# Kernel tuning notes

Measured on AMD Instinct MI355X. Metric: run time of the kernel, lower is better.

## Reference

```python
import jax, jax.numpy as jnp
import numpy as np

BETA = 0.25


def setup_inputs() -> dict:
    key = jax.random.key(0)
    k1, k2 = jax.random.split(key)
    z = jax.random.normal(k1, (16, 256, 32, 32), dtype=jnp.float32)
    n_e, e_dim = 8192, 256
    # torch init: uniform(-1/n_e, 1/n_e)
    codebook = jax.random.uniform(k2, (n_e, e_dim), dtype=jnp.float32,
                                  minval=-1.0 / n_e, maxval=1.0 / n_e)
    return {"z": z, "codebook": codebook}


def reference(z, codebook):
    # z: [B, C, H, W] -> [B, H, W, C]
    z_perm = jnp.transpose(z, (0, 2, 3, 1))
    B, H, W, C = z_perm.shape
    flat = z_perm.reshape(-1, C)  # [N, e_dim]
    distances = (jnp.sum(flat ** 2, axis=1, keepdims=True)
                 + jnp.sum(codebook ** 2, axis=1)
                 - 2.0 * jnp.matmul(flat, codebook.T))  # [N, n_e]
    indices = jnp.argmin(distances, axis=1)  # [N]
    quant = codebook[indices].reshape(z_perm.shape)  # [B, H, W, C]
    loss = (BETA * jnp.mean((jax.lax.stop_gradient(quant) - z_perm) ** 2)
            + jnp.mean((quant - jax.lax.stop_gradient(z_perm)) ** 2))
    # straight-through estimator
    quant = z_perm + jax.lax.stop_gradient(quant - z_perm)
    quant = jnp.transpose(quant, (0, 3, 1, 2))  # back to [B, C, H, W]
    return quant, loss, indices
```

## Files before the change

### kernel.cpp

```cpp
#include <hip/hip_runtime.h>
#include <stdint.h>

#define N_ROWS 16384
#define N_E    8192
#define EDIM   256
#define QELEMS 4194304
#define NCHUNK 256

using f32x4  = __attribute__((ext_vector_type(4))) float;
using bf16x8 = __attribute__((ext_vector_type(8))) short;

__device__ __forceinline__ unsigned int f2ord(float f) {
    unsigned int u = __float_as_uint(f);
    return (u & 0x80000000u) ? ~u : (u | 0x80000000u);
}
__device__ __forceinline__ float ord2f(unsigned int o) {
    unsigned int u = (o & 0x80000000u) ? (o & 0x7fffffffu) : ~o;
    return __uint_as_float(u);
}
__device__ __forceinline__ unsigned long long shfl_xor_u64(unsigned long long v, int m) {
    int lo = __shfl_xor((int)(unsigned int)(v & 0xffffffffull), m);
    int hi = __shfl_xor((int)(unsigned int)(v >> 32), m);
    return ((unsigned long long)(unsigned int)hi << 32) | (unsigned long long)(unsigned int)lo;
}
__device__ __forceinline__ unsigned short f2bf(float f) {
    unsigned int u = __float_as_uint(f);
    u += 0x7fffu + ((u >> 16) & 1u);
    return (unsigned short)(u >> 16);
}

__global__ void vq_rownorm(const float* __restrict__ z, float* __restrict__ Crow,
                           float* __restrict__ Mrow) {
    int r = blockIdx.x * blockDim.x + threadIdx.x;
    if (r >= N_ROWS) return;
    int b = r >> 10, hw = r & 1023;
    const float* p = z + ((size_t)b << 18) + hw;
    double s0 = 0.0, s1 = 0.0, s2 = 0.0, s3 = 0.0;
    float sa = 0.0f;
    #pragma unroll 4
    for (int c = 0; c < EDIM; c += 4) {
        float v0 = p[(size_t)(c + 0) << 10];
        float v1 = p[(size_t)(c + 1) << 10];
        float v2 = p[(size_t)(c + 2) << 10];
        float v3 = p[(size_t)(c + 3) << 10];
        float w0 = v0 * v0, w1 = v1 * v1, w2 = v2 * v2, w3 = v3 * v3;
        s0 += (double)w0; s1 += (double)w1; s2 += (double)w2; s3 += (double)w3;
        sa += fabsf(v0) + fabsf(v1) + fabsf(v2) + fabsf(v3);
    }
    Crow[r] = (float)((s0 + s1) + (s2 + s3));
    Mrow[r] = 1.6e-4f + 3.0e-6f * sa;
}

__global__ void vq_transpose(const float* __restrict__ z, float* __restrict__ Zt,
                             unsigned short* __restrict__ Zth) {
    __shared__ float tile[64][65];
    const int t = threadIdx.x;
    const int ct = blockIdx.x, rt = blockIdx.y;
    const int tr = t & 63, tc = t >> 6;
    #pragma unroll
    for (int i = 0; i < 16; ++i) {
        int c_l = i * 4 + tc;
        int r = rt * 64 + tr;
        int c = ct * 64 + c_l;
        tile[tr][c_l] = z[(((size_t)(r >> 10) * 256 + c) << 10) + (r & 1023)];
    }
    __syncthreads();
    const int c = ct * 64 + tr;
    const int kt = c >> 5, lkq = (c >> 3) & 3, k0 = c & 7;
    #pragma unroll
    for (int i = 0; i < 16; ++i) {
        int r_l = i * 4 + tc;
        int r = rt * 64 + r_l;
        float v = tile[r_l][tr];
        Zt[(size_t)r * EDIM + c] = v;
        size_t off = (((size_t)(r >> 4) * 8 + kt) * 64 + lkq * 16 + (r & 15)) * 8 + k0;
        Zth[off] = f2bf(v);
    }
}

__global__ void vq_cbsplit(const float* __restrict__ cb, unsigned short* __restrict__ cbh) {
    const int t = threadIdx.x;
    const int nt = blockIdx.x, ktb = blockIdx.y;
    const int nl0 = t >> 4, kq = t & 15;
    #pragma unroll
    for (int i = 0; i < 8; ++i) {
        int nl = i * 16 + nl0;
        int n = nt * 128 + nl;
        int k = ktb * 64 + kq * 4;
        float4 v = *(const float4*)(cb + (size_t)n * EDIM + k);
        ushort4 H;
        H.x = f2bf(v.x); H.y = f2bf(v.y); H.z = f2bf(v.z); H.w = f2bf(v.w);
        int kt = k >> 5, lkq = (k >> 3) & 3, k0 = k & 7;
        size_t off = (((size_t)(n >> 4) * 8 + kt) * 64 + lkq * 16 + (n & 15)) * 8 + k0;
        *(ushort4*)(cbh + off) = H;
    }
}

__global__ __launch_bounds__(512, 2) void vq_gemm(
    const unsigned short* __restrict__ Zth, const unsigned short* __restrict__ cbh,
    unsigned int* __restrict__ part)
{
    const int t = threadIdx.x;
    const int lane = t & 63, w = t >> 6;
    const int bid = blockIdx.x;
    const int rg0 = bid * 4;
    const int row0 = bid * 64;
    const unsigned short* gA = Zth + (size_t)lane * 8;
    const unsigned short* pB = cbh + (size_t)lane * 8;

    bf16x8 A[4][8];
    #pragma unroll
    for (int i = 0; i < 4; ++i)
        #pragma unroll
        for (int kt = 0; kt < 8; ++kt)
            A[i][kt] = *(const bf16x8*)(gA + (((size_t)(rg0 + i) * 8 + kt) << 9));

    const int cfw = w * 64;
    bf16x8 bc[8], bn[8];

#define LDB(dst, cf) { _Pragma("unroll") \
    for (int kt_ = 0; kt_ < 8; ++kt_) \
        (dst)[kt_] = *(const bf16x8*)(pB + (((size_t)(cf) * 8 + kt_) << 9)); }

    LDB(bc, cfw);

    #pragma unroll 1
    for (int ch = 0; ch < 32; ++ch) {
        #pragma unroll
        for (int i = 0; i < 4; ++i)
            #pragma unroll
            for (int kt = 0; kt < 8; ++kt)
                asm volatile("" : "+v"(A[i][kt]));

        const int gch = w * 32 + ch;
        f32x4 acc0[4], acc1[4];
        #pragma unroll
        for (int i = 0; i < 4; ++i) {
            acc0[i] = (f32x4){0.f, 0.f, 0.f, 0.f};
            acc1[i] = (f32x4){0.f, 0.f, 0.f, 0.f};
        }
        LDB(bn, cfw + ch * 2 + 1);
        __builtin_amdgcn_s_setprio(1);
        #pragma unroll
        for (int kt = 0; kt < 8; ++kt) {
            acc0[0] = __builtin_amdgcn_mfma_f32_16x16x32_bf16(bc[kt], A[0][kt], acc0[0], 0, 0, 0);
            acc0[1] = __builtin_amdgcn_mfma_f32_16x16x32_bf16(bc[kt], A[1][kt], acc0[1], 0, 0, 0);
            acc0[2] = __builtin_amdgcn_mfma_f32_16x16x32_bf16(bc[kt], A[2][kt], acc0[2], 0, 0, 0);
            acc0[3] = __builtin_amdgcn_mfma_f32_16x16x32_bf16(bc[kt], A[3][kt], acc0[3], 0, 0, 0);
        }
        __builtin_amdgcn_s_setprio(0);
        LDB(bc, (ch < 31) ? (cfw + ch * 2 + 2) : cfw);
        __builtin_amdgcn_s_setprio(1);
        #pragma unroll
        for (int kt = 0; kt < 8; ++kt) {
            acc1[0] = __builtin_amdgcn_mfma_f32_16x16x32_bf16(bn[kt], A[0][kt], acc1[0], 0, 0, 0);
            acc1[1] = __builtin_amdgcn_mfma_f32_16x16x32_bf16(bn[kt], A[1][kt], acc1[1], 0, 0, 0);
            acc1[2] = __builtin_amdgcn_mfma_f32_16x16x32_bf16(bn[kt], A[2][kt], acc1[2], 0, 0, 0);
            acc1[3] = __builtin_amdgcn_mfma_f32_16x16x32_bf16(bn[kt], A[3][kt], acc1[3], 0, 0, 0);
        }
        __builtin_amdgcn_s_setprio(0);
        #pragma unroll
        for (int i = 0; i < 4; ++i) {
            float m0 = fmaxf(acc0[i][0], acc1[i][0]);
            float m1 = fmaxf(acc0[i][1], acc1[i][1]);
            float m2 = fmaxf(acc0[i][2], acc1[i][2]);
            float m3 = fmaxf(acc0[i][3], acc1[i][3]);
            float v = fmaxf(fmaxf(m0, m1), fmaxf(m2, m3));
            v = fmaxf(v, __shfl_xor(v, 16));
            v = fmaxf(v, __shfl_xor(v, 32));
            if (lane < 16)
                part[(size_t)gch * N_ROWS + row0 + i * 16 + lane] = f2ord(v);
        }
    }
#undef LDB
}

__global__ void vq_qualify(const unsigned int* __restrict__ part,
                           const float* __restrict__ Mrow,
                           unsigned int* __restrict__ uthr)
{
    int row = blockIdx.x * 256 + threadIdx.x;
    unsigned int umax = 0u;
    for (int c = 0; c < NCHUNK; ++c) {
        unsigned int u = part[(size_t)c * N_ROWS + row];
        umax = (u > umax) ? u : umax;
    }
    float thr = ord2f(umax) - 0.5f * Mrow[row];
    uthr[row] = f2ord(thr);
}

__global__ __launch_bounds__(256, 1) void vq_recheck(
    const float* __restrict__ Zt, const float* __restrict__ cb,
    const float* __restrict__ Crow, const unsigned int* __restrict__ part,
    const unsigned int* __restrict__ uthr, unsigned long long* __restrict__ keys)
{
    __shared__ float cbt[32 * 256];
    __shared__ int lrows[N_ROWS];
    __shared__ int lcount;
    const int t = threadIdx.x;
    const int chunk = blockIdx.x;
    if (t == 0) lcount = 0;
    {
        int col = t >> 3, kq = t & 7;
        const float* src = cb + (size_t)(chunk * 32 + col) * EDIM + kq * 32;
        #pragma unroll
        for (int j = 0; j < 8; ++j) {
            float4 v = *(const float4*)(src + j * 4);
            int k4 = kq * 8 + j;
            *(float4*)&cbt[col * 256 + (((unsigned)(k4 ^ (col & 7))) << 2)] = v;
        }
    }
    __syncthreads();
    for (int r0 = 0; r0 < N_ROWS; r0 += 256) {
        int row = r0 + t;
        if (part[(size_t)chunk * N_ROWS + row] >= uthr[row]) {
            int pos = atomicAdd(&lcount, 1);
            lrows[pos] = row;
        }
    }
    __syncthreads();
    const int cnt = lcount;
    const int cg = t & 7, rl = t >> 3;
    for (int i0 = 0; i0 < cnt; i0 += 32) {
        int li = i0 + rl;
        bool valid = li < cnt;
        int row = lrows[valid ? li : (cnt - 1)];
        const float* zp = Zt + (size_t)row * EDIM;
        float a0 = 0.f, a1 = 0.f, a2 = 0.f, a3 = 0.f;
        #pragma unroll 8
        for (int k4 = 0; k4 < 64; ++k4) {
            float4 zv = *(const float4*)(zp + k4 * 4);
            int g = ((unsigned)(k4 ^ cg)) << 2;
            float4 b0 = *(const float4*)&cbt[(cg +  0) * 256 + g];
            float4 b1 = *(const float4*)&cbt[(cg +  8) * 256 + g];
            float4 b2 = *(const float4*)&cbt[(cg + 16) * 256 + g];
            float4 b3 = *(const float4*)&cbt[(cg + 24) * 256 + g];
            a0 = fmaf(zv.x, b0.x, a0); a0 = fmaf(zv.y, b0.y, a0);
            a0 = fmaf(zv.z, b0.z, a0); a0 = fmaf(zv.w, b0.w, a0);
            a1 = fmaf(zv.x, b1.x, a1); a1 = fmaf(zv.y, b1.y, a1);
            a1 = fmaf(zv.z, b1.z, a1); a1 = fmaf(zv.w, b1.w, a1);
            a2 = fmaf(zv.x, b2.x, a2); a2 = fmaf(zv.y, b2.y, a2);
            a2 = fmaf(zv.z, b2.z, a2); a2 = fmaf(zv.w, b2.w, a2);
            a3 = fmaf(zv.x, b3.x, a3); a3 = fmaf(zv.y, b3.y, a3);
            a3 = fmaf(zv.z, b3.z, a3); a3 = fmaf(zv.w, b3.w, a3);
        }
        float Cr = Crow[row];
        int colbase = chunk * 32;
        unsigned long long best;
        {
            unsigned long long k0 = ((unsigned long long)f2ord(Cr - 2.0f * a0) << 32) | (unsigned int)(colbase + cg);
            unsigned long long k1 = ((unsigned long long)f2ord(Cr - 2.0f * a1) << 32) | (unsigned int)(colbase + cg + 8);
            unsigned long long k2 = ((unsigned long long)f2ord(Cr - 2.0f * a2) << 32) | (unsigned int)(colbase + cg + 16);
            unsigned long long k3 = ((unsigned long long)f2ord(Cr - 2.0f * a3) << 32) | (unsigned int)(colbase + cg + 24);
            best = (k0 < k1) ? k0 : k1;
            best = (k2 < best) ? k2 : best;
            best = (k3 < best) ? k3 : best;
        }
        #pragma unroll
        for (int m = 1; m <= 4; m <<= 1) {
            unsigned long long o = shfl_xor_u64(best, m);
            best = (o < best) ? o : best;
        }
        if (cg == 0 && valid) atomicMin(&keys[row], best);
    }
}

__global__ void vq_finalize(const float* __restrict__ z, const float* __restrict__ cb,
                            const unsigned long long* __restrict__ keys,
                            float* __restrict__ out_q, float* __restrict__ out_idx,
                            double* __restrict__ accum)
{
    __shared__ float qld[64][257];
    __shared__ int sIdx[64];
    const int t = threadIdx.x;
    const int r0 = blockIdx.x * 64;
    const int b = r0 >> 10, hw0 = r0 & 1023;
    if (t < 64) {
        unsigned int idx = (unsigned int)(keys[r0 + t] & 0xffffffffull);
        sIdx[t] = (int)idx;
        out_idx[r0 + t] = (float)idx;
    }
    __syncthreads();
    {
        int i = t >> 2, q4 = t & 3;
        const float* src = cb + (size_t)sIdx[i] * EDIM;
        #pragma unroll
        for (int j = 0; j < 16; ++j)
            *(float4*)&qld[i][j * 16 + q4 * 4] = *(const float4*)(src + j * 16 + q4 * 4);
    }
    __syncthreads();
    const int hw_l = t & 63, cg = t >> 6;
    double p = 0.0;
    #pragma unroll 4
    for (int j = 0; j < 64; ++j) {
        int c = cg * 64 + j;
        float q  = qld[hw_l][c];
        size_t o = (((size_t)(b * 256 + c)) << 10) + hw0 + hw_l;
        float zv = z[o];
        float d  = q - zv;
        out_q[o] = zv + d;
        p += (double)d * (double)d;
    }
    #pragma unroll
    for (int m = 32; m >= 1; m >>= 1) p += __shfl_down(p, m);
    __shared__ double wsum[4];
    if ((t & 63) == 0) wsum[t >> 6] = p;
    __syncthreads();
    if (t == 0)
        atomicAdd(accum, (wsum[0] + wsum[1]) + (wsum[2] + wsum[3]));
}

__global__ void vq_loss(const double* __restrict__ accum, float* __restrict__ out_loss) {
    out_loss[0] = (float)(1.25 * (accum[0] / (double)QELEMS));
}

extern "C" void kernel_launch(void* const* d_in, const int* in_sizes, int n_in,
                              void* d_out, int out_size, void* d_ws, size_t ws_size,
                              hipStream_t stream) {
    const float* z  = (const float*)d_in[0];
    const float* cb = (const float*)d_in[1];
    float* out = (float*)d_out;

    char* ws = (char*)d_ws;
    unsigned long long* keys = (unsigned long long*)(ws + 0);
    float*  Crow  = (float*)(ws + 131072);
    float*  Mrow  = (float*)(ws + 196608);
    unsigned int* uthr = (unsigned int*)(ws + 262144);
    double* accum = (double*)(ws + 327680);
    unsigned int* part = (unsigned int*)(ws + 331776);
    float*  Zt    = (float*)(ws + 17108992);
    unsigned short* Zth = (unsigned short*)(ws + 33886208);
    unsigned short* cbh = (unsigned short*)(ws + 42274816);

    hipMemsetAsync(keys, 0xFF, (size_t)N_ROWS * 8, stream);
    hipMemsetAsync(accum, 0, 8, stream);

    vq_rownorm  <<<N_ROWS / 256, 256, 0, stream>>>(z, Crow, Mrow);
    vq_transpose<<<dim3(4, 256), 256, 0, stream>>>(z, Zt, Zth);
    vq_cbsplit  <<<dim3(64, 4), 256, 0, stream>>>(cb, cbh);
    vq_gemm     <<<256, 512, 0, stream>>>(Zth, cbh, part);
    vq_qualify  <<<N_ROWS / 256, 256, 0, stream>>>(part, Mrow, uthr);
    vq_recheck  <<<NCHUNK, 256, 0, stream>>>(Zt, cb, Crow, part, uthr, keys);
    vq_finalize <<<N_ROWS / 64, 256, 0, stream>>>(z, cb, keys, out, out + QELEMS + 1, accum);
    vq_loss     <<<1, 1, 0, stream>>>(accum, out + QELEMS);
}
```

Baseline: 183.0 us.

## Build per-chunk candidate lists in qualify and split recheck across four blocks per chunk

The qualify kernel now computes each row's threshold and scans all chunks, appending qualifying row indices as 16-bit values to per-chunk global lists through global atomics. Recheck no longer scans all 16384 rows per chunk into a 64KB shared list; it reads the prebuilt list and splits each chunk's candidates across four blocks, with a launch bound that allows three blocks per CU. This removes the per-chunk full scan of part/uthr and the heavy shared memory use, which should raise occupancy and parallelism. The cost is a second pass over part in qualify, contended global atomics on the per-chunk counters, and reuse of the Zth buffer for the lists after the GEMM has consumed it.

New measurement: 349.9 us. 1.91x slower.

```diff
diff --git a/kernel.cpp b/kernel.cpp
--- a/kernel.cpp
+++ b/kernel.cpp
@@ -177,7 +177,8 @@
 
 __global__ void vq_qualify(const unsigned int* __restrict__ part,
                            const float* __restrict__ Mrow,
-                           unsigned int* __restrict__ uthr)
+                           int* __restrict__ counts,
+                           unsigned short* __restrict__ lists16)
 {
     int row = blockIdx.x * 256 + threadIdx.x;
     unsigned int umax = 0u;
@@ -186,20 +187,24 @@
         umax = (u > umax) ? u : umax;
     }
     float thr = ord2f(umax) - 0.5f * Mrow[row];
-    uthr[row] = f2ord(thr);
-}
-
-__global__ __launch_bounds__(256, 1) void vq_recheck(
+    unsigned int uthrv = f2ord(thr);
+    for (int c = 0; c < NCHUNK; ++c)
+        if (part[(size_t)c * N_ROWS + row] >= uthrv) {
+            int pos = atomicAdd(&counts[c], 1);
+            lists16[(size_t)c * N_ROWS + pos] = (unsigned short)row;
+        }
+}
+
+__global__ __launch_bounds__(256, 3) void vq_recheck(
     const float* __restrict__ Zt, const float* __restrict__ cb,
-    const float* __restrict__ Crow, const unsigned int* __restrict__ part,
-    const unsigned int* __restrict__ uthr, unsigned long long* __restrict__ keys)
+    const float* __restrict__ Crow, const int* __restrict__ counts,
+    const unsigned short* __restrict__ lists16, unsigned long long* __restrict__ keys)
 {
     __shared__ float cbt[32 * 256];
-    __shared__ int lrows[N_ROWS];
-    __shared__ int lcount;
-    const int t = threadIdx.x;
-    const int chunk = blockIdx.x;
-    if (t == 0) lcount = 0;
+    const int t = threadIdx.x;
+    const int chunk = blockIdx.x >> 2, sub = blockIdx.x & 3;
+    const int cnt = counts[chunk];
+    if (cnt == 0 || sub * 32 >= cnt) return;
     {
         int col = t >> 3, kq = t & 7;
         const float* src = cb + (size_t)(chunk * 32 + col) * EDIM + kq * 32;
@@ -211,20 +216,12 @@
         }
     }
     __syncthreads();
-    for (int r0 = 0; r0 < N_ROWS; r0 += 256) {
-        int row = r0 + t;
-        if (part[(size_t)chunk * N_ROWS + row] >= uthr[row]) {
-            int pos = atomicAdd(&lcount, 1);
-            lrows[pos] = row;
-        }
-    }
-    __syncthreads();
-    const int cnt = lcount;
     const int cg = t & 7, rl = t >> 3;
-    for (int i0 = 0; i0 < cnt; i0 += 32) {
+    const unsigned short* lst = lists16 + (size_t)chunk * N_ROWS;
+    for (int i0 = sub * 32; i0 < cnt; i0 += 128) {
         int li = i0 + rl;
         bool valid = li < cnt;
-        int row = lrows[valid ? li : (cnt - 1)];
+        int row = lst[valid ? li : (cnt - 1)];
         const float* zp = Zt + (size_t)row * EDIM;
         float a0 = 0.f, a1 = 0.f, a2 = 0.f, a3 = 0.f;
         #pragma unroll 8
@@ -325,22 +322,24 @@
     unsigned long long* keys = (unsigned long long*)(ws + 0);
     float*  Crow  = (float*)(ws + 131072);
     float*  Mrow  = (float*)(ws + 196608);
-    unsigned int* uthr = (unsigned int*)(ws + 262144);
     double* accum = (double*)(ws + 327680);
+    int*    counts = (int*)(ws + 327688);
     unsigned int* part = (unsigned int*)(ws + 331776);
     float*  Zt    = (float*)(ws + 17108992);
     unsigned short* Zth = (unsigned short*)(ws + 33886208);
     unsigned short* cbh = (unsigned short*)(ws + 42274816);
+    unsigned short* lists16 = Zth;
 
     hipMemsetAsync(keys, 0xFF, (size_t)N_ROWS * 8, stream);
     hipMemsetAsync(accum, 0, 8, stream);
+    hipMemsetAsync(counts, 0, 1024, stream);
 
     vq_rownorm  <<<N_ROWS / 256, 256, 0, stream>>>(z, Crow, Mrow);
     vq_transpose<<<dim3(4, 256), 256, 0, stream>>>(z, Zt, Zth);
     vq_cbsplit  <<<dim3(64, 4), 256, 0, stream>>>(cb, cbh);
     vq_gemm     <<<256, 512, 0, stream>>>(Zth, cbh, part);
-    vq_qualify  <<<N_ROWS / 256, 256, 0, stream>>>(part, Mrow, uthr);
-    vq_recheck  <<<NCHUNK, 256, 0, stream>>>(Zt, cb, Crow, part, uthr, keys);
+    vq_qualify  <<<N_ROWS / 256, 256, 0, stream>>>(part, Mrow, counts, lists16);
+    vq_recheck  <<<NCHUNK * 4, 256, 0, stream>>>(Zt, cb, Crow, counts, lists16, keys);
     vq_finalize <<<N_ROWS / 64, 256, 0, stream>>>(z, cb, keys, out, out + QELEMS + 1, accum);
     vq_loss     <<<1, 1, 0, stream>>>(accum, out + QELEMS);
 }
```
